# Optimization experiments

Measured on AMD Instinct MI355X. Metric: run time of the kernel, lower is better.

## Reference

```python
import jax, jax.numpy as jnp
import numpy as np

H, D, BLK, R = 12, 64, 64, 3  # heads, size_per_head, block size, rand blocks
NEG = -1e9


def setup_inputs() -> dict:
    key = jax.random.key(0)
    ks = jax.random.split(key, 6)
    B, S, W = 2, 4096, H * D
    M = S // BLK
    return {
        "from_tensor": jax.random.normal(ks[0], (B, S, W), jnp.float32),
        "to_tensor": jax.random.normal(ks[1], (B, S, W), jnp.float32),
        "Wq": jax.random.normal(ks[2], (W, H * D), jnp.float32) * 0.02,
        "bq": jnp.zeros((H * D,), jnp.float32),
        "Wk": jax.random.normal(ks[3], (W, H * D), jnp.float32) * 0.02,
        "bk": jnp.zeros((H * D,), jnp.float32),
        "Wv": jax.random.normal(ks[4], (W, H * D), jnp.float32) * 0.02,
        "bv": jnp.zeros((H * D,), jnp.float32),
        "to_mask": jnp.ones((B, S), jnp.int32),
        "rand_attn": jax.random.randint(ks[5], (H, M - 2, R), 0, M - 2, jnp.int32),
    }


def _bigbird_block_sparse(from_tensor, to_tensor, Wq, bq, Wk, bk, Wv, bv, to_mask, rand_attn):
    B, S, _ = from_tensor.shape
    M = S // BLK
    scale = 1.0 / np.sqrt(D).astype(np.float32)

    # QKV projections -> [B,H,S,D]
    q = (from_tensor @ Wq + bq).reshape(B, S, H, D).transpose(0, 2, 1, 3)
    k = (to_tensor @ Wk + bk).reshape(B, S, H, D).transpose(0, 2, 1, 3)
    v = (to_tensor @ Wv + bv).reshape(B, S, H, D).transpose(0, 2, 1, 3)

    bq_ = q.reshape(B, H, M, BLK, D)
    bk_ = k.reshape(B, H, M, BLK, D)
    bv_ = v.reshape(B, H, M, BLK, D)

    tm = to_mask.astype(q.dtype)          # [B,S]
    bm = tm.reshape(B, M, BLK)            # [B,M,BLK]

    # gather random key/value blocks per head: [B,H,M-2,R*BLK,D]
    ha = jnp.arange(H)[:, None, None]
    gk = bk_[:, ha, rand_attn].reshape(B, H, M - 2, R * BLK, D)
    gv = bv_[:, ha, rand_attn].reshape(B, H, M - 2, R * BLK, D)
    gm = bm[:, rand_attn].reshape(B, H, M - 2, R * BLK)

    def full_row(qblk):  # first/last query blocks attend to everything
        s = jnp.einsum('bhqd,bhkd->bhqk', qblk, k) * scale + (1 - tm)[:, None, None, :] * NEG
        return jnp.einsum('bhqk,bhkd->bhqd', jax.nn.softmax(s, -1), v)

    def sparse_row(qblk, k_cat, v_cat, m_cat):  # [B,H,BLK,D] x [B,H,L,D]
        s = jnp.einsum('bhqd,bhkd->bhqk', qblk, k_cat) * scale + (1 - m_cat)[:, :, None, :] * NEG
        return jnp.einsum('bhqk,bhkd->bhqd', jax.nn.softmax(s, -1), v_cat)

    c_first = full_row(bq_[:, :, 0])
    c_last = full_row(bq_[:, :, M - 1])

    # second row: blocks [0,1,2,last] + rand
    k2 = jnp.concatenate([bk_[:, :, 0], bk_[:, :, 1], bk_[:, :, 2], bk_[:, :, M - 1], gk[:, :, 0]], axis=2)
    v2 = jnp.concatenate([bv_[:, :, 0], bv_[:, :, 1], bv_[:, :, 2], bv_[:, :, M - 1], gv[:, :, 0]], axis=2)
    m2s = jnp.concatenate([bm[:, 0], bm[:, 1], bm[:, 2], bm[:, M - 1]], axis=-1)
    m2 = jnp.concatenate([jnp.broadcast_to(m2s[:, None], (B, H, 4 * BLK)), gm[:, :, 0]], axis=-1)
    c_second = sparse_row(bq_[:, :, 1], k2, v2, m2)

    # second-to-last row: blocks [0,M-3,M-2,M-1] + rand
    k3 = jnp.concatenate([bk_[:, :, 0], bk_[:, :, M - 3], bk_[:, :, M - 2], bk_[:, :, M - 1], gk[:, :, M - 3]], axis=2)
    v3 = jnp.concatenate([bv_[:, :, 0], bv_[:, :, M - 3], bv_[:, :, M - 2], bv_[:, :, M - 1], gv[:, :, M - 3]], axis=2)
    m3s = jnp.concatenate([bm[:, 0], bm[:, M - 3], bm[:, M - 2], bm[:, M - 1]], axis=-1)
    m3 = jnp.concatenate([jnp.broadcast_to(m3s[:, None], (B, H, 4 * BLK)), gm[:, :, M - 3]], axis=-1)
    c_secondlast = sparse_row(bq_[:, :, M - 2], k3, v3, m3)

    # middle rows 2..M-3: band(prev,self,next) + rand + global first/last blocks
    L = M - 4
    band_k = jnp.concatenate([bk_[:, :, 1:M - 3], bk_[:, :, 2:M - 2], bk_[:, :, 3:M - 1]], axis=3)  # [B,H,L,3BLK,D]
    band_v = jnp.concatenate([bv_[:, :, 1:M - 3], bv_[:, :, 2:M - 2], bv_[:, :, 3:M - 1]], axis=3)
    band_m = jnp.concatenate([bm[:, 1:M - 3], bm[:, 2:M - 2], bm[:, 3:M - 1]], axis=-1)  # [B,L,3BLK]

    k_mid = jnp.concatenate([
        band_k, gk[:, :, 1:M - 3],
        jnp.broadcast_to(bk_[:, :, 0:1], (B, H, L, BLK, D)),
        jnp.broadcast_to(bk_[:, :, M - 1:M], (B, H, L, BLK, D))], axis=3)
    v_mid = jnp.concatenate([
        band_v, gv[:, :, 1:M - 3],
        jnp.broadcast_to(bv_[:, :, 0:1], (B, H, L, BLK, D)),
        jnp.broadcast_to(bv_[:, :, M - 1:M], (B, H, L, BLK, D))], axis=3)
    m_mid = jnp.concatenate([
        jnp.broadcast_to(band_m[:, None], (B, H, L, 3 * BLK)),
        gm[:, :, 1:M - 3],
        jnp.broadcast_to(bm[:, None, None, 0], (B, H, L, BLK)),
        jnp.broadcast_to(bm[:, None, None, M - 1], (B, H, L, BLK))], axis=-1)

    s_mid = jnp.einsum('bhlqd,bhlkd->bhlqk', bq_[:, :, 2:M - 2], k_mid) * scale
    s_mid = s_mid + (1 - m_mid)[:, :, :, None, :] * NEG
    c_mid = jnp.einsum('bhlqk,bhlkd->bhlqd', jax.nn.softmax(s_mid, -1), v_mid)

    ctx = jnp.concatenate([
        c_first[:, :, None], c_second[:, :, None], c_mid,
        c_secondlast[:, :, None], c_last[:, :, None]], axis=2)  # [B,H,M,BLK,D]
    return ctx.reshape(B, H, S, D).transpose(0, 2, 1, 3)  # [B,S,H,D]


def reference(from_tensor, to_tensor, Wq, bq, Wk, bk, Wv, bv, to_mask, rand_attn):
    return _bigbird_block_sparse(from_tensor, to_tensor, Wq, bq, Wk, bk, Wv, bv, to_mask, rand_attn)
```

## Files before the change

### kernel.cpp

```cpp
#include <hip/hip_runtime.h>

typedef __attribute__((ext_vector_type(4))) float f32x4;
typedef __attribute__((ext_vector_type(8))) __bf16 bf16x8;
typedef __attribute__((ext_vector_type(8))) unsigned short u16x8;
typedef __attribute__((ext_vector_type(4))) unsigned short u16x4;

__device__ __forceinline__ unsigned short f2bf(float f) {
  unsigned u = __builtin_bit_cast(unsigned, f);
  u += 0x7fffu + ((u >> 16) & 1u);
  return (unsigned short)(u >> 16);
}

__device__ __forceinline__ f32x4 mfma16(bf16x8 a, bf16x8 b, f32x4 c) {
  return __builtin_amdgcn_mfma_f32_16x16x32_bf16(a, b, c, 0, 0, 0);
}

__device__ __forceinline__ void gload_lds16(const void* g, void* l) {
  __builtin_amdgcn_global_load_lds(
      (const __attribute__((address_space(1))) void*)g,
      (__attribute__((address_space(3))) void*)l, 16, 0, 0);
}

#define NQK 6291456
#define NX 6291456
#define NW 589824

__global__ __launch_bounds__(256) void prep_kernel(
    const float* __restrict__ Wq, const float* __restrict__ Wk,
    const float* __restrict__ Wv, const float* __restrict__ from_t,
    const float* __restrict__ to_t, unsigned short* __restrict__ Wt,
    unsigned short* __restrict__ xb) {
  __shared__ float tile[64][65];
  const int bid = blockIdx.x;
  const int t = threadIdx.x;
  if (bid < 432) {
    const int z = bid / 144, rest = bid % 144;
    const float* __restrict__ src = (z == 0) ? Wq : (z == 1) ? Wk : Wv;
    unsigned short* __restrict__ dst = Wt + (size_t)z * NW;
    const int k0 = (rest / 12) * 64, n0 = (rest % 12) * 64;
    const int r = t >> 4, c4 = (t & 15) * 4;
#pragma unroll
    for (int p = 0; p < 4; ++p) {
      int rr = r + p * 16;
      f32x4 v = *(const f32x4*)(src + (size_t)(k0 + rr) * 768 + n0 + c4);
#pragma unroll
      for (int j = 0; j < 4; ++j) tile[rr][c4 + j] = v[j];
    }
    __syncthreads();
#pragma unroll
    for (int p = 0; p < 4; ++p) {
      int rn = r + p * 16;
      u16x4 o;
#pragma unroll
      for (int j = 0; j < 4; ++j) o[j] = f2bf(tile[c4 + j][rn]);
      *(u16x4*)(dst + (size_t)(n0 + rn) * 768 + k0 + c4) = o;
    }
  } else {
    const int idx = bid - 432;
    const int y = idx / 3072, xi = idx % 3072;
    const float* __restrict__ src = y ? to_t : from_t;
    unsigned short* __restrict__ dst = xb + (size_t)y * NX;
    const size_t i = ((size_t)xi * 256 + t) * 8;
    f32x4 a = *(const f32x4*)(src + i);
    f32x4 b = *(const f32x4*)(src + i + 4);
    u16x8 o;
#pragma unroll
    for (int j = 0; j < 4; ++j) { o[j] = f2bf(a[j]); o[j + 4] = f2bf(b[j]); }
    *(u16x8*)(dst + i) = o;
  }
}

__global__ __launch_bounds__(256) void qkv_gemm_kernel(
    const unsigned short* __restrict__ Xb, const unsigned short* __restrict__ Wt,
    const float* __restrict__ bq, const float* __restrict__ bk,
    const float* __restrict__ bv, unsigned short* __restrict__ qkvQK,
    unsigned short* __restrict__ vt, int zoff, int cpx) {
  __shared__ unsigned short A_lds[2][8192];
  __shared__ unsigned short B_lds[2][8192];
  const int bid0 = blockIdx.x;
  const int bid = (bid0 & 7) * cpx + (bid0 >> 3);
  const int z = zoff + bid / 384;
  const int rem = bid % 384;
  const int bn = rem >> 6, bm = rem & 63;
  const unsigned short* __restrict__ X = Xb + (z ? (size_t)NX : 0);
  const unsigned short* __restrict__ Wz = Wt + (size_t)z * NW;
  const float* __restrict__ bias = (z == 0) ? bq : (z == 1) ? bk : bv;
  const int t = threadIdx.x, lane = t & 63, w = t >> 6;
  const int wm = (w >> 1) * 64, wn = (w & 1) * 64;
  const int l15 = lane & 15, cc = lane >> 4;

  f32x4 acc[4][4];
#pragma unroll
  for (int i = 0; i < 4; ++i)
#pragma unroll
    for (int j = 0; j < 4; ++j) acc[i][j] = (f32x4){0.f, 0.f, 0.f, 0.f};

  const unsigned short* Abase = X + (size_t)bm * 128 * 768;
  const unsigned short* Bbase = Wz + (size_t)bn * 128 * 768;

  auto STAGE = [&](int ks, int bufi) {
#pragma unroll
    for (int p = 0; p < 4; ++p) {
      int wb = p * 4 + w;
      int ch = wb * 64 + lane;
      int r = ch >> 3, sl = ch & 7;
      int g = sl ^ (r & 7);
      gload_lds16(Abase + (size_t)r * 768 + ks * 64 + g * 8,
                  &A_lds[bufi][wb * 512]);
      gload_lds16(Bbase + (size_t)r * 768 + ks * 64 + g * 8,
                  &B_lds[bufi][wb * 512]);
    }
  };

  STAGE(0, 0);
  __syncthreads();

  for (int ks = 0; ks < 12; ++ks) {
    const int cur = ks & 1;
    if (ks < 11) STAGE(ks + 1, cur ^ 1);

    bf16x8 af[4][2], bfr[4][2];
#pragma unroll
    for (int mi = 0; mi < 4; ++mi) {
      int row = wm + mi * 16 + l15;
      const char* rp = (const char*)A_lds[cur] + row * 128;
#pragma unroll
      for (int kk = 0; kk < 2; ++kk)
        af[mi][kk] = *(const bf16x8*)(rp + (((cc + 4 * kk) ^ (row & 7)) << 4));
    }
#pragma unroll
    for (int ni = 0; ni < 4; ++ni) {
      int row = wn + ni * 16 + l15;
      const char* rp = (const char*)B_lds[cur] + row * 128;
#pragma unroll
      for (int kk = 0; kk < 2; ++kk)
        bfr[ni][kk] = *(const bf16x8*)(rp + (((cc + 4 * kk) ^ (row & 7)) << 4));
    }
#pragma unroll
    for (int kk = 0; kk < 2; ++kk)
#pragma unroll
      for (int mi = 0; mi < 4; ++mi)
#pragma unroll
        for (int ni = 0; ni < 4; ++ni)
          acc[mi][ni] = mfma16(af[mi][kk], bfr[ni][kk], acc[mi][ni]);
    __syncthreads();
  }

  if (z < 2) {
    const float qscale = (z == 0) ? 0.125f : 1.0f;
    unsigned short* __restrict__ dst = qkvQK + (size_t)z * NQK;
#pragma unroll
    for (int ni = 0; ni < 4; ++ni) {
      int gn = bn * 128 + wn + ni * 16 + l15;
      float bv_ = bias[gn];
      int hh = gn >> 6, dd = gn & 63;
#pragma unroll
      for (int mi = 0; mi < 4; ++mi) {
#pragma unroll
        for (int r = 0; r < 4; ++r) {
          int gm = bm * 128 + wm + mi * 16 + cc * 4 + r;
          int bb = gm >> 12, s = gm & 4095;
          float val = (acc[mi][ni][r] + bv_) * qscale;
          dst[((((size_t)bb * 12 + hh) * 4096 + s) * 64) + dd] = f2bf(val);
        }
      }
    }
  } else {
#pragma unroll
    for (int ni = 0; ni < 4; ++ni) {
      int gn = bn * 128 + wn + ni * 16 + l15;
      float bv_ = bias[gn];
      int hh = gn >> 6, dd = gn & 63;
#pragma unroll
      for (int mi = 0; mi < 4; ++mi) {
        int gm0 = bm * 128 + wm + mi * 16 + cc * 4;
        int bb = gm0 >> 12, s0 = gm0 & 4095;
        u16x4 o;
#pragma unroll
        for (int r = 0; r < 4; ++r) o[r] = f2bf(acc[mi][ni][r] + bv_);
        *(u16x4*)(vt + ((size_t)(bb * 12 + hh) * 64 + dd) * 4096 + s0) = o;
      }
    }
  }
}

__global__ __launch_bounds__(256) void attn_kernel(
    const unsigned short* __restrict__ qkvQK, const unsigned short* __restrict__ vt,
    const int* __restrict__ to_mask, const int* __restrict__ rand_attn,
    float* __restrict__ out, float* __restrict__ part_o,
    float* __restrict__ part_ml) {
  __shared__ unsigned short K_lds[2][4096];
  __shared__ unsigned short VT_lds[2][4096];
  __shared__ unsigned short P_lds[4][1024];
  __shared__ float penal[8][64];
  __shared__ int blist[8];

  const int bid0 = blockIdx.x;
  const int bid = (bid0 & 7) * 234 + (bid0 >> 3);
  const int bh = bid / 78, r78 = bid % 78;
  const int h = bh % 12, b = bh / 12;
  const int t = threadIdx.x, lane = t & 63, w = t >> 6;
  const int l15 = lane & 15, cc = lane >> 4;

  int m, nblk, chunk = 0;
  bool full;
  if (r78 < 62) {
    full = false;
    m = r78 + 1;
    nblk = (m == 1 || m == 62) ? 7 : 8;
    if (t == 0) {
      const int* rp = rand_attn + ((size_t)h * 62 + (m - 1)) * 3;
      if (m == 1) {
        blist[0] = 0; blist[1] = 1; blist[2] = 2; blist[3] = 63;
        blist[4] = rp[0]; blist[5] = rp[1]; blist[6] = rp[2];
      } else if (m == 62) {
        blist[0] = 0; blist[1] = 61; blist[2] = 62; blist[3] = 63;
        blist[4] = rp[0]; blist[5] = rp[1]; blist[6] = rp[2];
      } else {
        blist[0] = m - 1; blist[1] = m; blist[2] = m + 1;
        blist[3] = rp[0]; blist[4] = rp[1]; blist[5] = rp[2];
        blist[6] = 0; blist[7] = 63;
      }
    }
  } else {
    full = true;
    int fr = r78 - 62;
    chunk = fr & 7;
    m = (fr >> 3) ? 63 : 0;
    nblk = 8;
    if (t < 8) blist[t] = chunk * 8 + t;
  }

  const unsigned short* qp = qkvQK + (((size_t)b * 12 + h) * 4096 + m * 64) * 64;
  const unsigned short* kp = qkvQK + NQK + (((size_t)b * 12 + h) * 4096) * 64;
  const unsigned short* vtp = vt + (((size_t)b * 12 + h) * 64) * 4096;

  int loff[2];
  const unsigned short *kpl[2], *vpl[2];
#pragma unroll
  for (int p = 0; p < 2; ++p) {
    int wb = p * 4 + w;
    int ch = wb * 64 + lane;
    int rr = ch >> 3;
    int g = (ch & 7) ^ (rr & 7);
    loff[p] = wb * 512;
    kpl[p] = kp + rr * 64 + g * 8;
    vpl[p] = vtp + rr * 4096 + g * 8;
  }

  bf16x8 aq[2];
  {
    int qrow = w * 16 + l15;
    aq[0] = *(const bf16x8*)(qp + qrow * 64 + cc * 8);
    aq[1] = *(const bf16x8*)(qp + qrow * 64 + 32 + cc * 8);
  }

  float m_run = -INFINITY, l_run = 0.f;
  f32x4 o_acc[4];
#pragma unroll
  for (int dg = 0; dg < 4; ++dg) o_acc[dg] = (f32x4){0.f, 0.f, 0.f, 0.f};

  char* pw = (char*)P_lds[w];
  const int swz = (l15 & 7) << 4;

  auto STAGE = [&](int kb, int bufi) {
    const size_t ko = (size_t)kb * 4096;
    const size_t vo = (size_t)kb * 64;
    gload_lds16(kpl[0] + ko, &K_lds[bufi][loff[0]]);
    gload_lds16(kpl[1] + ko, &K_lds[bufi][loff[1]]);
    gload_lds16(vpl[0] + vo, &VT_lds[bufi][loff[0]]);
    gload_lds16(vpl[1] + vo, &VT_lds[bufi][loff[1]]);
  };

  __syncthreads();

  {
    int ib = w;
#pragma unroll
    for (int pp = 0; pp < 2; ++pp, ib += 4)
      if (ib < nblk)
        penal[ib][lane] =
            (1.0f - (float)to_mask[(size_t)b * 4096 + blist[ib] * 64 + lane]) *
            (-1e9f);
  }
  STAGE(blist[0], 0);
  __syncthreads();

  for (int ib = 0; ib < nblk; ++ib) {
    const int cur = ib & 1;
    if (ib + 1 < nblk) STAGE(blist[ib + 1], cur ^ 1);

    float sm[4][4];
    const char* kbase = (const char*)K_lds[cur];
    __builtin_amdgcn_s_setprio(1);
#pragma unroll
    for (int kg = 0; kg < 4; ++kg) {
      int krow = kg * 16 + l15;
      const char* rp = kbase + krow * 128;
      int sz = (krow & 7) << 4;
      bf16x8 k0 = *(const bf16x8*)(rp + ((cc << 4) ^ sz));
      bf16x8 k1 = *(const bf16x8*)(rp + (((cc + 4) << 4) ^ sz));
      f32x4 zz = (f32x4){0.f, 0.f, 0.f, 0.f};
      zz = mfma16(k0, aq[0], zz);
      zz = mfma16(k1, aq[1], zz);
      f32x4 pen = *(const f32x4*)(&penal[ib][kg * 16 + cc * 4]);
#pragma unroll
      for (int r = 0; r < 4; ++r) sm[kg][r] = zz[r] + pen[r];
    }
    __builtin_amdgcn_s_setprio(0);

    float mx = sm[0][0];
#pragma unroll
    for (int kg = 0; kg < 4; ++kg)
#pragma unroll
      for (int r = 0; r < 4; ++r) mx = fmaxf(mx, sm[kg][r]);
    mx = fmaxf(mx, __shfl_xor(mx, 16, 64));
    mx = fmaxf(mx, __shfl_xor(mx, 32, 64));

    if (__any(mx > m_run)) {
      float mn = fmaxf(m_run, mx);
      float fac = __expf(m_run - mn);
      m_run = mn;
      l_run *= fac;
      float fr_[4];
#pragma unroll
      for (int r = 0; r < 4; ++r) fr_[r] = __shfl(fac, cc * 4 + r, 64);
#pragma unroll
      for (int dg = 0; dg < 4; ++dg)
#pragma unroll
        for (int r = 0; r < 4; ++r) o_acc[dg][r] *= fr_[r];
    }

    float rs = 0.f;
    u16x4 pb[4];
#pragma unroll
    for (int kg = 0; kg < 4; ++kg)
#pragma unroll
      for (int r = 0; r < 4; ++r) {
        float p = __expf(sm[kg][r] - m_run);
        rs += p;
        pb[kg][r] = f2bf(p);
      }
    rs += __shfl_xor(rs, 16, 64);
    rs += __shfl_xor(rs, 32, 64);
    l_run += rs;

#pragma unroll
    for (int kg = 0; kg < 4; ++kg)
      *(u16x4*)(pw + l15 * 128 + ((kg * 32 + cc * 8) ^ swz)) = pb[kg];
    __builtin_amdgcn_wave_barrier();
    bf16x8 ap0 = *(const bf16x8*)(pw + l15 * 128 + ((cc << 4) ^ swz));
    bf16x8 ap1 = *(const bf16x8*)(pw + l15 * 128 + (((cc + 4) << 4) ^ swz));

    const char* vbase = (const char*)VT_lds[cur];
    __builtin_amdgcn_s_setprio(1);
#pragma unroll
    for (int dg = 0; dg < 4; ++dg) {
      int drow = dg * 16 + l15;
      const char* vb = vbase + drow * 128;
      int sz = (drow & 7) << 4;
      bf16x8 v0 = *(const bf16x8*)(vb + ((cc << 4) ^ sz));
      bf16x8 v1 = *(const bf16x8*)(vb + (((cc + 4) << 4) ^ sz));
      o_acc[dg] = mfma16(ap0, v0, o_acc[dg]);
      o_acc[dg] = mfma16(ap1, v1, o_acc[dg]);
    }
    __builtin_amdgcn_s_setprio(0);
    __syncthreads();
  }

  if (!full) {
    float inv[4];
#pragma unroll
    for (int r = 0; r < 4; ++r) inv[r] = 1.0f / __shfl(l_run, cc * 4 + r, 64);
#pragma unroll
    for (int r = 0; r < 4; ++r) {
      int s = m * 64 + w * 16 + cc * 4 + r;
#pragma unroll
      for (int dg = 0; dg < 4; ++dg) {
        int d = dg * 16 + l15;
        out[(((size_t)b * 4096 + s) * 12 + h) * 64 + d] = o_acc[dg][r] * inv[r];
      }
    }
  } else {
    const int row = (b * 12 + h) * 2 + (m ? 1 : 0);
    float* po = part_o + (((size_t)row * 8 + chunk) * 64) * 64;
    float* pml = part_ml + ((size_t)row * 8 + chunk) * 128;
#pragma unroll
    for (int r = 0; r < 4; ++r) {
      int q = w * 16 + cc * 4 + r;
#pragma unroll
      for (int dg = 0; dg < 4; ++dg) {
        int d = dg * 16 + l15;
        po[q * 64 + d] = o_acc[dg][r];
      }
    }
    if (cc == 0) {
      pml[w * 16 + l15] = m_run;
      pml[64 + w * 16 + l15] = l_run;
    }
  }
}

__global__ __launch_bounds__(256) void combine_kernel(
    const float* __restrict__ part_o, const float* __restrict__ part_ml,
    float* __restrict__ out) {
  const int row = blockIdx.x;
  const int b = row / 24, h = (row >> 1) % 12, m = (row & 1) ? 63 : 0;
  const int t = threadIdx.x;
  const int q = t >> 2, d0 = (t & 3) * 16;

  float mc[8], lc[8];
  float M = -INFINITY;
#pragma unroll
  for (int c = 0; c < 8; ++c) {
    const float* pml = part_ml + ((size_t)row * 8 + c) * 128;
    mc[c] = pml[q];
    lc[c] = pml[64 + q];
    M = fmaxf(M, mc[c]);
  }
  float wgt[8], L = 0.f;
#pragma unroll
  for (int c = 0; c < 8; ++c) {
    wgt[c] = __expf(mc[c] - M);
    L += wgt[c] * lc[c];
  }
  f32x4 acc[4];
#pragma unroll
  for (int j = 0; j < 4; ++j) acc[j] = (f32x4){0.f, 0.f, 0.f, 0.f};
#pragma unroll
  for (int c = 0; c < 8; ++c) {
    const float* po = part_o + (((size_t)row * 8 + c) * 64 + q) * 64 + d0;
#pragma unroll
    for (int j = 0; j < 4; ++j) {
      f32x4 v = *(const f32x4*)(po + j * 4);
#pragma unroll
      for (int e = 0; e < 4; ++e) acc[j][e] += wgt[c] * v[e];
    }
  }
  const float inv = 1.0f / L;
  const int s = m * 64 + q;
  float* op = out + (((size_t)b * 4096 + s) * 12 + h) * 64 + d0;
#pragma unroll
  for (int j = 0; j < 4; ++j) {
    f32x4 v;
#pragma unroll
    for (int e = 0; e < 4; ++e) v[e] = acc[j][e] * inv;
    *(f32x4*)(op + j * 4) = v;
  }
}

extern "C" void kernel_launch(void* const* d_in, const int* in_sizes, int n_in,
                              void* d_out, int out_size, void* d_ws,
                              size_t ws_size, hipStream_t stream) {
  (void)in_sizes; (void)n_in; (void)out_size; (void)ws_size;
  const float* from_t = (const float*)d_in[0];
  const float* to_t = (const float*)d_in[1];
  const float* Wq = (const float*)d_in[2];
  const float* bq = (const float*)d_in[3];
  const float* Wk = (const float*)d_in[4];
  const float* bk = (const float*)d_in[5];
  const float* Wv = (const float*)d_in[6];
  const float* bv = (const float*)d_in[7];
  const int* to_mask = (const int*)d_in[8];
  const int* rand_attn = (const int*)d_in[9];
  float* out = (float*)d_out;

  unsigned short* Wt = (unsigned short*)d_ws;
  unsigned short* qkvQK = Wt + (size_t)3 * NW;
  unsigned short* Xb = qkvQK + (size_t)2 * NQK;
  unsigned short* vt = Xb;
  float* part_o = (float*)(Xb + (size_t)NX);
  float* part_ml = part_o + (size_t)48 * 8 * 64 * 64;

  prep_kernel<<<dim3(6576), dim3(256), 0, stream>>>(Wq, Wk, Wv, from_t, to_t,
                                                    Wt, Xb);
  qkv_gemm_kernel<<<dim3(768), dim3(256), 0, stream>>>(
      Xb, Wt, bq, bk, bv, qkvQK, vt, 0, 96);
  qkv_gemm_kernel<<<dim3(384), dim3(256), 0, stream>>>(
      Xb, Wt, bq, bk, bv, qkvQK, vt, 2, 48);
  attn_kernel<<<dim3(1872), dim3(256), 0, stream>>>(
      qkvQK, vt, to_mask, rand_attn, out, part_o, part_ml);
  combine_kernel<<<dim3(48), dim3(256), 0, stream>>>(part_o, part_ml, out);
}
```

Measured before the change: 124.0 us.

## Use exp2 softmax, lazy rescale, packed bf16 cvt, and single QKV GEMM launch

Folds log2(e) into the Q scale and the mask penalty so the softmax can use exp2f instead of __expf. The online-softmax rescale now only runs when the running max grows by more than 8, instead of on every increase. The bf16 probabilities are packed with v_cvt_pk_bf16_f32, and the max and sum reductions are tree-shaped. When the workspace is large enough, V gets its own buffer so all three projections run in a single 1152-block GEMM launch instead of two, and the GEMM tile order is changed to be N-inner. This adds a workspace-size-dependent code path, and the lazy rescale relies on bounded exponent growth to avoid overflow.

```diff
diff --git a/kernel.cpp b/kernel.cpp
--- a/kernel.cpp
+++ b/kernel.cpp
@@ -4,11 +4,20 @@
 typedef __attribute__((ext_vector_type(8))) __bf16 bf16x8;
 typedef __attribute__((ext_vector_type(8))) unsigned short u16x8;
 typedef __attribute__((ext_vector_type(4))) unsigned short u16x4;
+typedef __attribute__((ext_vector_type(2))) unsigned int u32x2;
+
+#define LOG2E 1.4426950408889634f
 
 __device__ __forceinline__ unsigned short f2bf(float f) {
   unsigned u = __builtin_bit_cast(unsigned, f);
   u += 0x7fffu + ((u >> 16) & 1u);
   return (unsigned short)(u >> 16);
+}
+
+__device__ __forceinline__ unsigned cvtpk(float lo, float hi) {
+  unsigned r;
+  asm("v_cvt_pk_bf16_f32 %0, %1, %2" : "=v"(r) : "v"(lo), "v"(hi));
+  return r;
 }
 
 __device__ __forceinline__ f32x4 mfma16(bf16x8 a, bf16x8 b, f32x4 c) {
@@ -81,7 +90,7 @@
   const int bid = (bid0 & 7) * cpx + (bid0 >> 3);
   const int z = zoff + bid / 384;
   const int rem = bid % 384;
-  const int bn = rem >> 6, bm = rem & 63;
+  const int bm = rem / 6, bn = rem % 6;
   const unsigned short* __restrict__ X = Xb + (z ? (size_t)NX : 0);
   const unsigned short* __restrict__ Wz = Wt + (size_t)z * NW;
   const float* __restrict__ bias = (z == 0) ? bq : (z == 1) ? bk : bv;
@@ -147,7 +156,7 @@
   }
 
   if (z < 2) {
-    const float qscale = (z == 0) ? 0.125f : 1.0f;
+    const float qscale = (z == 0) ? 0.125f * LOG2E : 1.0f;
     unsigned short* __restrict__ dst = qkvQK + (size_t)z * NQK;
 #pragma unroll
     for (int ni = 0; ni < 4; ++ni) {
@@ -281,7 +290,7 @@
       if (ib < nblk)
         penal[ib][lane] =
             (1.0f - (float)to_mask[(size_t)b * 4096 + blist[ib] * 64 + lane]) *
-            (-1e9f);
+            (-1e9f * LOG2E);
   }
   STAGE(blist[0], 0);
   __syncthreads();
@@ -309,17 +318,17 @@
     }
     __builtin_amdgcn_s_setprio(0);
 
-    float mx = sm[0][0];
+    float mk[4];
 #pragma unroll
     for (int kg = 0; kg < 4; ++kg)
-#pragma unroll
-      for (int r = 0; r < 4; ++r) mx = fmaxf(mx, sm[kg][r]);
+      mk[kg] = fmaxf(fmaxf(sm[kg][0], sm[kg][1]), fmaxf(sm[kg][2], sm[kg][3]));
+    float mx = fmaxf(fmaxf(mk[0], mk[1]), fmaxf(mk[2], mk[3]));
     mx = fmaxf(mx, __shfl_xor(mx, 16, 64));
     mx = fmaxf(mx, __shfl_xor(mx, 32, 64));
 
-    if (__any(mx > m_run)) {
+    if (!__all(mx - m_run <= 8.0f)) {
       float mn = fmaxf(m_run, mx);
-      float fac = __expf(m_run - mn);
+      float fac = exp2f(m_run - mn);
       m_run = mn;
       l_run *= fac;
       float fr_[4];
@@ -331,23 +340,27 @@
         for (int r = 0; r < 4; ++r) o_acc[dg][r] *= fr_[r];
     }
 
-    float rs = 0.f;
-    u16x4 pb[4];
+    float p_[4][4];
 #pragma unroll
     for (int kg = 0; kg < 4; ++kg)
 #pragma unroll
-      for (int r = 0; r < 4; ++r) {
-        float p = __expf(sm[kg][r] - m_run);
-        rs += p;
-        pb[kg][r] = f2bf(p);
-      }
+      for (int r = 0; r < 4; ++r) p_[kg][r] = exp2f(sm[kg][r] - m_run);
+    float ss[4];
+#pragma unroll
+    for (int kg = 0; kg < 4; ++kg)
+      ss[kg] = (p_[kg][0] + p_[kg][1]) + (p_[kg][2] + p_[kg][3]);
+    float rs = (ss[0] + ss[1]) + (ss[2] + ss[3]);
     rs += __shfl_xor(rs, 16, 64);
     rs += __shfl_xor(rs, 32, 64);
     l_run += rs;
 
 #pragma unroll
-    for (int kg = 0; kg < 4; ++kg)
-      *(u16x4*)(pw + l15 * 128 + ((kg * 32 + cc * 8) ^ swz)) = pb[kg];
+    for (int kg = 0; kg < 4; ++kg) {
+      u32x2 wv;
+      wv[0] = cvtpk(p_[kg][0], p_[kg][1]);
+      wv[1] = cvtpk(p_[kg][2], p_[kg][3]);
+      *(u32x2*)(pw + l15 * 128 + ((kg * 32 + cc * 8) ^ swz)) = wv;
+    }
     __builtin_amdgcn_wave_barrier();
     bf16x8 ap0 = *(const bf16x8*)(pw + l15 * 128 + ((cc << 4) ^ swz));
     bf16x8 ap1 = *(const bf16x8*)(pw + l15 * 128 + (((cc + 4) << 4) ^ swz));
@@ -421,7 +434,7 @@
   float wgt[8], L = 0.f;
 #pragma unroll
   for (int c = 0; c < 8; ++c) {
-    wgt[c] = __expf(mc[c] - M);
+    wgt[c] = exp2f(mc[c] - M);
     L += wgt[c] * lc[c];
   }
   f32x4 acc[4];
@@ -452,7 +465,7 @@
 extern "C" void kernel_launch(void* const* d_in, const int* in_sizes, int n_in,
                               void* d_out, int out_size, void* d_ws,
                               size_t ws_size, hipStream_t stream) {
-  (void)in_sizes; (void)n_in; (void)out_size; (void)ws_size;
+  (void)in_sizes; (void)n_in; (void)out_size;
   const float* from_t = (const float*)d_in[0];
   const float* to_t = (const float*)d_in[1];
   const float* Wq = (const float*)d_in[2];
@@ -468,17 +481,36 @@
   unsigned short* Wt = (unsigned short*)d_ws;
   unsigned short* qkvQK = Wt + (size_t)3 * NW;
   unsigned short* Xb = qkvQK + (size_t)2 * NQK;
-  unsigned short* vt = Xb;
-  float* part_o = (float*)(Xb + (size_t)NX);
-  float* part_ml = part_o + (size_t)48 * 8 * 64 * 64;
-
-  prep_kernel<<<dim3(6576), dim3(256), 0, stream>>>(Wq, Wk, Wv, from_t, to_t,
-                                                    Wt, Xb);
-  qkv_gemm_kernel<<<dim3(768), dim3(256), 0, stream>>>(
-      Xb, Wt, bq, bk, bv, qkvQK, vt, 0, 96);
-  qkv_gemm_kernel<<<dim3(384), dim3(256), 0, stream>>>(
-      Xb, Wt, bq, bk, bv, qkvQK, vt, 2, 48);
-  attn_kernel<<<dim3(1872), dim3(256), 0, stream>>>(
-      qkvQK, vt, to_mask, rand_attn, out, part_o, part_ml);
-  combine_kernel<<<dim3(48), dim3(256), 0, stream>>>(part_o, part_ml, out);
-}
+
+  const size_t part_elems = (size_t)48 * 8 * 64 * 64 + (size_t)48 * 8 * 128;
+  const size_t fused_bytes =
+      ((size_t)3 * NW + 2 * NQK + 2 * NX + NQK) * 2 + part_elems * 4;
+
+  if (ws_size >= fused_bytes) {
+    unsigned short* vt = Xb + (size_t)2 * NX;
+    float* part_o = (float*)Xb;
+    float* part_ml = part_o + (size_t)48 * 8 * 64 * 64;
+
+    prep_kernel<<<dim3(6576), dim3(256), 0, stream>>>(Wq, Wk, Wv, from_t, to_t,
+                                                      Wt, Xb);
+    qkv_gemm_kernel<<<dim3(1152), dim3(256), 0, stream>>>(
+        Xb, Wt, bq, bk, bv, qkvQK, vt, 0, 144);
+    attn_kernel<<<dim3(1872), dim3(256), 0, stream>>>(
+        qkvQK, vt, to_mask, rand_attn, out, part_o, part_ml);
+    combine_kernel<<<dim3(48), dim3(256), 0, stream>>>(part_o, part_ml, out);
+  } else {
+    unsigned short* vt = Xb;
+    float* part_o = (float*)(Xb + (size_t)NX);
+    float* part_ml = part_o + (size_t)48 * 8 * 64 * 64;
+
+    prep_kernel<<<dim3(6576), dim3(256), 0, stream>>>(Wq, Wk, Wv, from_t, to_t,
+                                                      Wt, Xb);
+    qkv_gemm_kernel<<<dim3(768), dim3(256), 0, stream>>>(
+        Xb, Wt, bq, bk, bv, qkvQK, vt, 0, 96);
+    qkv_gemm_kernel<<<dim3(384), dim3(256), 0, stream>>>(
+        Xb, Wt, bq, bk, bv, qkvQK, vt, 2, 48);
+    attn_kernel<<<dim3(1872), dim3(256), 0, stream>>>(
+        qkvQK, vt, to_mask, rand_attn, out, part_o, part_ml);
+    combine_kernel<<<dim3(48), dim3(256), 0, stream>>>(part_o, part_ml, out);
+  }
+}
```

Measured after the change: 115.1 us. 1.08x faster.
